# Kernel optimization log

Measured on AMD Instinct MI355X. Metric: run time of the kernel, lower is better.

The kernel has to match this reference:

```python
import jax, jax.numpy as jnp
import numpy as np
from functools import partial

NUM_HEADS = 12
RATIO_ACT = 0.5   # prune_ratio_act_store
RATIO_ATTN = 0.5  # prune_ratio_attn_mat_store


def kth_mask(x, ratio):
    # torch.kthvalue semantics: threshold = k-th SMALLEST of |x| over the flat tensor
    n = x.size
    k = int(np.clip(n * ratio, 1, n))
    mag = jnp.abs(x)
    thr = jnp.sort(mag.reshape(-1))[k - 1]
    return (mag >= thr).astype(x.dtype)


def st(dense, prune):
    # straight-through: value = dense, gradient flows through `prune` path
    return jax.lax.stop_gradient(dense) + prune - jax.lax.stop_gradient(prune)


def _softmax_prune_impl(x, ratio):
    dense = jax.nn.softmax(x, axis=-1)
    mask = kth_mask(dense, ratio)
    return dense, mask * dense


@partial(jax.custom_vjp, nondiff_argnums=(1,))
def softmax_prune(x, ratio):
    return _softmax_prune_impl(x, ratio)


def _sp_fwd(x, ratio):
    dense, sparse = _softmax_prune_impl(x, ratio)
    return (dense, sparse), sparse


def _sp_bwd(ratio, A, cots):
    # custom backward uses the SPARSE probs in the softmax Jacobian; the
    # cotangent of the sparse output is ignored (matches the torch Function)
    g_dense, _ = cots
    g = A * (g_dense - jnp.sum(g_dense * A, axis=-1, keepdims=True))
    return (g,)


softmax_prune.defvjp(_sp_fwd, _sp_bwd)


def setup_inputs() -> dict:
    key = jax.random.key(0)
    ks = jax.random.split(key, 5)
    B, S, H = 8, 577, 768
    hs = jax.random.normal(ks[0], (B, S, H), dtype=jnp.float32)
    w = lambda k: jax.random.normal(k, (H, H), dtype=jnp.float32) * 0.02
    z = jnp.zeros((H,), dtype=jnp.float32)
    return {
        "hidden_states": hs,
        "Wq": w(ks[1]), "bq": z,
        "Wk": w(ks[2]), "bk": z,
        "Wv": w(ks[3]), "bv": z,
        "Wo": w(ks[4]), "bo": z,
    }


def attention_forward(hidden_states, Wq, bq, Wk, bk, Wv, bv, Wo, bo):
    B, S, H = hidden_states.shape
    nh, hd = NUM_HEADS, H // NUM_HEADS
    sg = jax.lax.stop_gradient
    lin = lambda x, W, b: x @ W + b

    # prune hidden states by global magnitude threshold
    hs_p = sg(kth_mask(hidden_states, RATIO_ACT)) * hidden_states

    q = st(lin(hidden_states, Wq, bq), lin(hs_p, Wq, bq))
    k = st(lin(hidden_states, Wk, bk), lin(hs_p, Wk, bk))
    v = st(lin(hidden_states, Wv, bv), lin(hs_p, Wv, bv))

    heads = lambda x: x.reshape(B, S, nh, hd).transpose(0, 2, 1, 3)  # [B,h,S,d]
    q, k, v = heads(q), heads(k), heads(v)

    qp = sg(kth_mask(q, RATIO_ACT)) * q
    kp = sg(kth_mask(k, RATIO_ACT)) * k

    scores = st(jnp.einsum('bhqd,bhkd->bhqk', q, k),
                jnp.einsum('bhqd,bhkd->bhqk', qp, kp))
    scores = scores / float(np.sqrt(hd))

    probs, probs_p = softmax_prune(scores, RATIO_ATTN)  # dropout rate = 0 -> identity

    vp = sg(kth_mask(v, RATIO_ACT)) * v
    ctx = st(jnp.einsum('bhqk,bhkd->bhqd', probs, v),
             jnp.einsum('bhqk,bhkd->bhqd', probs_p, vp))

    ctx = ctx.transpose(0, 2, 1, 3).reshape(B, S, H)
    ctx_p = sg(kth_mask(ctx, RATIO_ACT)) * ctx

    out = st(lin(ctx, Wo, bo), lin(ctx_p, Wo, bo))
    return out  # vis=False -> weights is None


def reference(hidden_states, Wq, bq, Wk, bk, Wv, bv, Wo, bo):
    return attention_forward(hidden_states, Wq, bq, Wk, bk, Wv, bv, Wo, bo)
```

## Files before the change

### kernel.cpp

```cpp
#include <hip/hip_runtime.h>
#include <hip/hip_bf16.h>


#define B_ 8
#define S_ 577
#define H_ 768
#define NH_ 12
#define HD_ 64
#define M_ (B_*S_)
#define MPAD 4736
#define BH_ (B_*NH_)
#define SKPAD 640
#define LTS 136

typedef __attribute__((ext_vector_type(8))) short short8;
typedef __attribute__((ext_vector_type(4))) short s16x4;
typedef __attribute__((ext_vector_type(4))) float f32x4;

__device__ inline unsigned short f2bf(float f){
    unsigned int u = __float_as_uint(f);
    u = u + 0x7fffu + ((u>>16)&1u);
    return (unsigned short)(u>>16);
}

__device__ inline void gload_lds16(const short* g, short* l){
    __builtin_amdgcn_global_load_lds((const __attribute__((address_space(1))) void*)g,
                                     (__attribute__((address_space(3))) void*)l, 16, 0, 0);
}

__global__ __launch_bounds__(256) void k_prep(
    const float* __restrict__ hs, short* __restrict__ abf,
    const float* __restrict__ Wq, const float* __restrict__ Wk,
    const float* __restrict__ Wv, const float* __restrict__ Wo,
    short* __restrict__ Tq, short* __restrict__ Tk,
    short* __restrict__ Tv, short* __restrict__ To,
    short* __restrict__ kh, short* __restrict__ vt)
{
    const int bid = blockIdx.x, t = threadIdx.x;
    if(bid < 1776){
        int i = bid*256 + t;
        if(bid >= 1731){ *(short8*)(abf + (size_t)i*8) = (short8){}; return; }
        const float4* p = (const float4*)(hs + (size_t)i*8);
        float4 a = p[0], b = p[1];
        short8 v;
        v[0]=(short)f2bf(a.x); v[1]=(short)f2bf(a.y); v[2]=(short)f2bf(a.z); v[3]=(short)f2bf(a.w);
        v[4]=(short)f2bf(b.x); v[5]=(short)f2bf(b.y); v[6]=(short)f2bf(b.z); v[7]=(short)f2bf(b.w);
        *(short8*)(abf + (size_t)i*8) = v;
    } else if(bid < 2352){
        int zidx = bid - 1776;
        int z = zidx & 3, rem = zidx >> 2;
        int kx = rem % 12, ny = rem / 12;
        const float* W = z==0?Wq: z==1?Wk: z==2?Wv:Wo;
        short*       T = z==0?Tq: z==1?Tk: z==2?Tv:To;
        __shared__ float lds[64][65];
        int k0 = kx*64, n0 = ny*64;
        for(int i=0;i<4;i++){
            int row = i*16 + (t>>4);
            int col = (t&15)*4;
            float4 v = *(const float4*)&W[(k0+row)*768 + n0 + col];
            lds[row][col]=v.x; lds[row][col+1]=v.y; lds[row][col+2]=v.z; lds[row][col+3]=v.w;
        }
        __syncthreads();
        for(int i=0;i<4;i++){
            int n = i*16 + (t>>4);
            int k4 = (t&15)*4;
            for(int j=0;j<4;j++)
                T[(n0+n)*768 + k0 + k4 + j] = (short)f2bf(lds[k4+j][n]);
        }
    } else {
        int tid = (bid-2352)*256 + t;
        short8 z = {};
        if(tid < 48384){
            int row_id = tid>>3, ch = tid&7;
            int bh = row_id/63, r = row_id - bh*63;
            *(short8*)&kh[((size_t)bh*SKPAD + 577 + r)*64 + ch*8] = z;
        } else if(tid < 97536){
            int j = tid - 48384;
            int row_id = j>>3, ch = j&7;
            int bh = row_id>>6, d = row_id&63;
            *(short8*)&vt[((size_t)bh*64 + d)*SKPAD + 576 + ch*8] = z;
        }
    }
}

__global__ __launch_bounds__(512) void k_gemm(
    const short* __restrict__ A, const short* __restrict__ T,
    const float* __restrict__ b0, const float* __restrict__ b1, const float* __restrict__ b2,
    short* __restrict__ oq, short* __restrict__ ok, short* __restrict__ ovt,
    float* __restrict__ of, int mode, int NT)
{
    __shared__ short sh[32768];
    const int t = threadIdx.x;

    const int nwg = gridDim.x;
    const int q8 = nwg>>3, r8 = nwg&7;
    const int xcd = blockIdx.x&7, cidx = blockIdx.x>>3;
    const int wg = (xcd<r8 ? xcd*(q8+1) : r8*(q8+1) + (xcd-r8)*q8) + cidx;
    const int mt = wg/NT, ntile = wg - mt*NT;
    const int m0 = mt*128, n0 = ntile*128;

    const int seg = (mode==3)? 0 : n0/768;
    const float* bias = (mode==3)? b0 : (seg==0?b0: seg==1?b1:b2);
    const int nlb = (mode==3)? n0 : n0 - seg*768;

    const int w = t>>6, lane = t&63, g = lane>>4, c = lane&15;
    const int wm = w>>1, wn = w&1;

    const int lrow = lane>>3;
    const int lcol = ((lane&7) ^ lrow) * 8;
    const short* pa = A + (size_t)(m0 + w*8 + lrow)*768 + lcol;
    const short* pb = T + (size_t)(n0 + w*8 + lrow)*768 + lcol;

    f32x4 acc[2][4] = {};

    #pragma unroll
    for(int i=0;i<2;i++){
        gload_lds16(pa + (size_t)(i*64)*768, &sh[(i*64 + w*8)*64]);
        gload_lds16(pb + (size_t)(i*64)*768, &sh[8192 + (i*64 + w*8)*64]);
    }
    int bb = 0;
    for(int kk=0; kk<12; kk++){
        if(kk<11){
            short* dstA = &sh[(bb^1)*16384];
            short* dstB = dstA + 8192;
            #pragma unroll
            for(int i=0;i<2;i++){
                gload_lds16(pa + (size_t)(i*64)*768 + (kk+1)*64, &dstA[(i*64 + w*8)*64]);
                gload_lds16(pb + (size_t)(i*64)*768 + (kk+1)*64, &dstB[(i*64 + w*8)*64]);
            }
            asm volatile("s_waitcnt vmcnt(4)" ::: "memory");
        } else {
            asm volatile("s_waitcnt vmcnt(0)" ::: "memory");
        }
        __builtin_amdgcn_s_barrier();
        asm volatile("" ::: "memory");

        const short* LA = &sh[bb*16384];
        const short* LB = LA + 8192;
        short8 af[2][2], bfv[4][2];
        #pragma unroll
        for(int mi=0; mi<2; mi++){
            int row = wm*32 + mi*16 + c;
            int rx = (row&7)<<3;
            af[mi][0] = *(const short8*)&LA[row*64 + ((g*8) ^ rx)];
            af[mi][1] = *(const short8*)&LA[row*64 + ((32 + g*8) ^ rx)];
        }
        #pragma unroll
        for(int ni=0; ni<4; ni++){
            int row = wn*64 + ni*16 + c;
            int rx = (row&7)<<3;
            bfv[ni][0] = *(const short8*)&LB[row*64 + ((g*8) ^ rx)];
            bfv[ni][1] = *(const short8*)&LB[row*64 + ((32 + g*8) ^ rx)];
        }
        __builtin_amdgcn_s_setprio(1);
        #pragma unroll
        for(int mi=0; mi<2; mi++)
            #pragma unroll
            for(int ni=0; ni<4; ni++){
                acc[mi][ni] = __builtin_amdgcn_mfma_f32_16x16x32_bf16(af[mi][0], bfv[ni][0], acc[mi][ni], 0,0,0);
                acc[mi][ni] = __builtin_amdgcn_mfma_f32_16x16x32_bf16(af[mi][1], bfv[ni][1], acc[mi][ni], 0,0,0);
            }
        __builtin_amdgcn_s_setprio(0);
        asm volatile("s_waitcnt lgkmcnt(0)" ::: "memory");
        __builtin_amdgcn_s_barrier();
        asm volatile("" ::: "memory");
        bb ^= 1;
    }

    if(mode==3){
        #pragma unroll
        for(int mi=0; mi<2; mi++) for(int ni=0; ni<4; ni++){
            #pragma unroll
            for(int r=0; r<4; r++){
                int m = m0 + wm*32 + mi*16 + g*4 + r;
                int n = n0 + wn*64 + ni*16 + c;
                if(m >= M_) continue;
                of[(size_t)m*768 + n] = acc[mi][ni][r] + bias[n];
            }
        }
        return;
    }

    if(seg==2){
        #pragma unroll
        for(int mi=0;mi<2;mi++)
            #pragma unroll
            for(int ni=0;ni<4;ni++){
                int nl_ = wn*64 + ni*16 + c;
                float bv = bias[nlb + nl_];
                s16x4 pk;
                #pragma unroll
                for(int r=0;r<4;r++) pk[r] = (short)f2bf(acc[mi][ni][r] + bv);
                int ml0 = wm*32 + mi*16 + g*4;
                *(s16x4*)&sh[nl_*LTS + ml0] = pk;
            }
    } else {
        #pragma unroll
        for(int mi=0;mi<2;mi++)
            #pragma unroll
            for(int ni=0;ni<4;ni++){
                int nl_ = wn*64 + ni*16 + c;
                float bv = bias[nlb + nl_];
                #pragma unroll
                for(int r=0;r<4;r++){
                    int ml = wm*32 + mi*16 + g*4 + r;
                    sh[ml*LTS + nl_] = (short)f2bf(acc[mi][ni][r] + bv);
                }
            }
    }
    __syncthreads();

    #pragma unroll
    for(int i=0;i<4;i++){
        int idx = i*512 + t;
        int rp = idx>>4, ch = idx&15;
        short8 v8 = *(const short8*)&sh[rp*LTS + ch*8];
        if(seg==2){
            int nl = nlb + rp, hh = nl>>6, dd = nl&63;
            int mg = m0 + ch*8;
            if(mg < M_){
                int b0_ = mg/S_, s0 = mg - b0_*S_;
                if(s0+7 < S_ && mg+7 < M_){
                    *(short8*)&ovt[(((size_t)b0_*NH_+hh)*HD_+dd)*SKPAD + s0] = v8;
                } else {
                    for(int j=0;j<8;j++){
                        int m=mg+j;
                        if(m<M_){ int bj=m/S_, sj=m-bj*S_;
                            ovt[(((size_t)bj*NH_+hh)*HD_+dd)*SKPAD+sj]=v8[j]; }
                    }
                }
            }
        } else {
            int m = m0 + rp;
            if(m < M_){
                int b0_ = m/S_, s0 = m - b0_*S_;
                int nl = nlb + ch*8, hh = nl>>6, dd = nl&63;
                if(seg==1) *(short8*)&ok[(((size_t)b0_*NH_+hh)*SKPAD + s0)*HD_ + dd] = v8;
                else       *(short8*)&oq[(((size_t)b0_*NH_+hh)*S_   + s0)*HD_ + dd] = v8;
            }
        }
    }
}

__global__ __launch_bounds__(256) void k_attn(
    const short* __restrict__ qh, const short* __restrict__ kh, const short* __restrict__ vt,
    short* __restrict__ ctx)
{
    __shared__ short lP[4*2048];
    const int t = threadIdx.x;
    const int w = t>>6, lane = t&63, g = lane>>4, c = lane&15;
    const int bh = blockIdx.x, b = bh/NH_, h = bh%NH_;
    const int q0 = blockIdx.y*128;

    #pragma unroll
    for(int i=0;i<4;i++){
        int row = i*8 + (lane>>3);
        int e8 = (lane&7)*8;
        int s = q0 + w*32 + row;
        short8 v = {};
        if(s < S_) v = *(const short8*)&qh[((size_t)bh*S_ + s)*HD_ + e8];
        *(short8*)&lP[w*2048 + row*64 + (e8 ^ ((row&7)<<3))] = v;
    }
    short8 qf[2][2];
    #pragma unroll
    for(int qi=0; qi<2; qi++)
        #pragma unroll
        for(int ks=0; ks<2; ks++)
            qf[qi][ks] = *(const short8*)&lP[w*2048 + (qi*16+c)*64 + ((ks*32+g*8) ^ ((c&7)<<3))];

    short8 ones;
    #pragma unroll
    for(int j=0;j<8;j++) ones[j] = (short)0x3F80;

    const short* Kb = kh + (size_t)bh*SKPAD*64 + (size_t)c*64 + g*8;
    const short* Vb = vt + (size_t)bh*64*SKPAD + (size_t)c*SKPAD + g*8;

    float m_run[2][4], l_run[2][4];
    f32x4 O[2][4] = {};
    #pragma unroll
    for(int qi=0;qi<2;qi++)
        #pragma unroll
        for(int r=0;r<4;r++){ m_run[qi][r] = -3e38f; l_run[qi][r] = 0.f; }

    #pragma unroll 1
    for(int kt=0; kt<10; kt++){
        const int key0 = kt*64;
        short8 kf[4][2], vf[4][2];
        #pragma unroll
        for(int nt=0; nt<4; nt++){
            const short* kr = Kb + (size_t)(key0 + nt*16)*64;
            kf[nt][0] = *(const short8*)(kr);
            kf[nt][1] = *(const short8*)(kr + 32);
            const short* vr = Vb + (size_t)(nt*16)*SKPAD + key0;
            vf[nt][0] = *(const short8*)(vr);
            vf[nt][1] = *(const short8*)(vr + 32);
        }

        float sv[2][4][4];
        #pragma unroll
        for(int nt=0; nt<4; nt++){
            __builtin_amdgcn_s_setprio(1);
            #pragma unroll
            for(int qi=0; qi<2; qi++){
                f32x4 sa = {};
                sa = __builtin_amdgcn_mfma_f32_16x16x32_bf16(qf[qi][0], kf[nt][0], sa, 0,0,0);
                sa = __builtin_amdgcn_mfma_f32_16x16x32_bf16(qf[qi][1], kf[nt][1], sa, 0,0,0);
                #pragma unroll
                for(int r=0;r<4;r++) sv[qi][nt][r] = sa[r]*0.18033688011f;
            }
            __builtin_amdgcn_s_setprio(0);
        }
        if(kt==9){
            #pragma unroll
            for(int nt=0; nt<4; nt++){
                int key = 576 + nt*16 + c;
                if(key >= S_){
                    #pragma unroll
                    for(int qi=0;qi<2;qi++)
                        #pragma unroll
                        for(int r=0;r<4;r++) sv[qi][nt][r] = -3e38f;
                }
            }
        }
        float fac[2][4];
        #pragma unroll
        for(int qi=0; qi<2; qi++)
            #pragma unroll
            for(int r=0;r<4;r++){
                float mx = fmaxf(fmaxf(sv[qi][0][r],sv[qi][1][r]),fmaxf(sv[qi][2][r],sv[qi][3][r]));
                for(int off=1; off<16; off<<=1) mx = fmaxf(mx, __shfl_xor(mx, off));
                float nm = fmaxf(m_run[qi][r], mx);
                fac[qi][r] = __builtin_amdgcn_exp2f(m_run[qi][r] - nm);
                m_run[qi][r] = nm;
            }
        #pragma unroll
        for(int qi=0; qi<2; qi++)
            #pragma unroll
            for(int nt=0; nt<4; nt++)
                #pragma unroll
                for(int r=0;r<4;r++){
                    float p = __builtin_amdgcn_exp2f(sv[qi][nt][r] - m_run[qi][r]);
                    int prow = g*4 + r;
                    lP[w*2048 + qi*1024 + prow*64 + ((nt*16 + c) ^ ((prow&7)<<3))] = (short)f2bf(p);
                }
        short8 pf[2][2];
        #pragma unroll
        for(int qi=0; qi<2; qi++)
            #pragma unroll
            for(int ks=0; ks<2; ks++)
                pf[qi][ks] = *(const short8*)&lP[w*2048 + qi*1024 + c*64 + ((ks*32+g*8) ^ ((c&7)<<3))];
        __builtin_amdgcn_s_setprio(1);
        #pragma unroll
        for(int qi=0; qi<2; qi++){
            f32x4 rs = {};
            rs = __builtin_amdgcn_mfma_f32_16x16x32_bf16(pf[qi][0], ones, rs, 0,0,0);
            rs = __builtin_amdgcn_mfma_f32_16x16x32_bf16(pf[qi][1], ones, rs, 0,0,0);
            #pragma unroll
            for(int r=0;r<4;r++) l_run[qi][r] = l_run[qi][r]*fac[qi][r] + rs[r];
        }
        __builtin_amdgcn_s_setprio(0);
        #pragma unroll
        for(int qi=0; qi<2; qi++)
            #pragma unroll
            for(int nt=0;nt<4;nt++)
                #pragma unroll
                for(int r=0;r<4;r++) O[qi][nt][r] *= fac[qi][r];

        __builtin_amdgcn_s_setprio(1);
        #pragma unroll
        for(int nt=0; nt<4; nt++)
            #pragma unroll
            for(int qi=0; qi<2; qi++){
                O[qi][nt] = __builtin_amdgcn_mfma_f32_16x16x32_bf16(pf[qi][0], vf[nt][0], O[qi][nt], 0,0,0);
                O[qi][nt] = __builtin_amdgcn_mfma_f32_16x16x32_bf16(pf[qi][1], vf[nt][1], O[qi][nt], 0,0,0);
            }
        __builtin_amdgcn_s_setprio(0);
    }

    #pragma unroll
    for(int qi=0; qi<2; qi++)
        #pragma unroll
        for(int nt=0; nt<4; nt++)
            #pragma unroll
            for(int r=0;r<4;r++){
                int s = q0 + w*32 + qi*16 + g*4 + r;
                if(s < S_){
                    float val = O[qi][nt][r] / l_run[qi][r];
                    ctx[((size_t)b*S_ + s)*H_ + h*HD_ + nt*16 + c] = (short)f2bf(val);
                }
            }
}

extern "C" void kernel_launch(void* const* d_in, const int* in_sizes, int n_in,
                              void* d_out, int out_size, void* d_ws, size_t ws_size,
                              hipStream_t stream)
{
    const float* hs = (const float*)d_in[0];
    const float* Wq = (const float*)d_in[1];
    const float* bq = (const float*)d_in[2];
    const float* Wk = (const float*)d_in[3];
    const float* bk = (const float*)d_in[4];
    const float* Wv = (const float*)d_in[5];
    const float* bv = (const float*)d_in[6];
    const float* Wo = (const float*)d_in[7];
    const float* bo = (const float*)d_in[8];
    float* out = (float*)d_out;

    char* ws = (char*)d_ws;
    short* abf = (short*)(ws);
    short* ctx = abf;
    short* wqt = (short*)(ws + 7274496);
    short* wkt = (short*)(ws + 7274496 + 1179648);
    short* wvt = (short*)(ws + 7274496 + 2*1179648);
    short* wot = (short*)(ws + 7274496 + 3*1179648);
    short* qh  = (short*)(ws + 11993088);
    short* kh  = (short*)(ws + 19083264);
    short* vt  = (short*)(ws + 26947584);

    k_prep<<<2733, 256, 0, stream>>>(hs, abf, Wq,Wk,Wv,Wo, wqt,wkt,wvt,wot, kh, vt);
    k_gemm<<<666, 512, 0, stream>>>(abf, wqt, bq,bk,bv, qh,kh,vt, nullptr, 0, 18);
    k_attn<<<dim3(96,5), 256, 0, stream>>>(qh, kh, vt, ctx);
    k_gemm<<<222, 512, 0, stream>>>(ctx, wot, bo,bo,bo, nullptr,nullptr,nullptr, out, 3, 6);
}
```

Measured before the change: 102.3 us.

## Stage K/V tiles in double-buffered LDS with async global-to-LDS loads

The attention kernel now loads 128-key K and V tiles cooperatively into shared LDS with direct global-to-LDS loads. It double-buffers them so the next tile is fetched while the current one is computed, and the key loop drops from ten 64-key steps to five 128-key steps. The aim is to cut redundant per-wave global loads of K/V, since all four waves previously fetched the same data, and to hide memory latency. The cost is about 80KB of LDS per block plus extra barriers, which may lower occupancy.

```diff
diff --git a/kernel.cpp b/kernel.cpp
--- a/kernel.cpp
+++ b/kernel.cpp
@@ -246,7 +246,7 @@
     const short* __restrict__ qh, const short* __restrict__ kh, const short* __restrict__ vt,
     short* __restrict__ ctx)
 {
-    __shared__ short lP[4*2048];
+    __shared__ short lK[2][128*64], lV[2][64*128], lP[4*2048];
     const int t = threadIdx.x;
     const int w = t>>6, lane = t&63, g = lane>>4, c = lane&15;
     const int bh = blockIdx.x, b = bh/NH_, h = bh%NH_;
@@ -272,8 +272,22 @@
     #pragma unroll
     for(int j=0;j<8;j++) ones[j] = (short)0x3F80;
 
-    const short* Kb = kh + (size_t)bh*SKPAD*64 + (size_t)c*64 + g*8;
-    const short* Vb = vt + (size_t)bh*64*SKPAD + (size_t)c*SKPAD + g*8;
+    const short* pk[4]; const short* pv[4]; int dk[4], dv[4];
+    #pragma unroll
+    for(int i=0;i<4;i++){
+        int id = i*256 + t;
+        int krow = id>>3, kch = id&7;
+        pk[i] = kh + ((size_t)bh*SKPAD + krow)*64 + (kch ^ (krow&7))*8;
+        dk[i] = krow*64 + kch*8;
+        int vd = id>>4, vch = id&15;
+        pv[i] = vt + ((size_t)bh*64 + vd)*SKPAD + (vch ^ (vd&7))*8;
+        dv[i] = vd*128 + vch*8;
+    }
+    #define STAGE(kt) { _Pragma("unroll") for(int i_=0;i_<4;i_++){           \
+        gload_lds16(pk[i_] + (size_t)(kt)*8192, &lK[(kt)&1][dk[i_]]);        \
+        gload_lds16(pv[i_] + (kt)*128,          &lV[(kt)&1][dv[i_]]); } }
+
+    STAGE(0);
 
     float m_run[2][4], l_run[2][4];
     f32x4 O[2][4] = {};
@@ -282,100 +296,99 @@
         #pragma unroll
         for(int r=0;r<4;r++){ m_run[qi][r] = -3e38f; l_run[qi][r] = 0.f; }
 
-    #pragma unroll 1
-    for(int kt=0; kt<10; kt++){
-        const int key0 = kt*64;
-        short8 kf[4][2], vf[4][2];
-        #pragma unroll
-        for(int nt=0; nt<4; nt++){
-            const short* kr = Kb + (size_t)(key0 + nt*16)*64;
-            kf[nt][0] = *(const short8*)(kr);
-            kf[nt][1] = *(const short8*)(kr + 32);
-            const short* vr = Vb + (size_t)(nt*16)*SKPAD + key0;
-            vf[nt][0] = *(const short8*)(vr);
-            vf[nt][1] = *(const short8*)(vr + 32);
-        }
-
-        float sv[2][4][4];
-        #pragma unroll
-        for(int nt=0; nt<4; nt++){
-            __builtin_amdgcn_s_setprio(1);
-            #pragma unroll
-            for(int qi=0; qi<2; qi++){
+    for(int kt=0; kt<5; kt++){
+        if(kt<4){
+            STAGE(kt+1);
+            asm volatile("s_waitcnt vmcnt(8)" ::: "memory");
+        } else {
+            asm volatile("s_waitcnt vmcnt(0)" ::: "memory");
+        }
+        __builtin_amdgcn_s_barrier();
+        asm volatile("" ::: "memory");
+
+        const short* LK = lK[kt&1]; const short* LV = lV[kt&1];
+
+        #pragma unroll
+        for(int qi=0; qi<2; qi++){
+            float sv[8][4];
+            #pragma unroll
+            for(int nt=0; nt<8; nt++){
+                int row = nt*16 + c;
+                int rx = (row&7)<<3;
+                short8 kf0 = *(const short8*)&LK[row*64 + ((g*8) ^ rx)];
+                short8 kf1 = *(const short8*)&LK[row*64 + ((32+g*8) ^ rx)];
+                __builtin_amdgcn_s_setprio(1);
                 f32x4 sa = {};
-                sa = __builtin_amdgcn_mfma_f32_16x16x32_bf16(qf[qi][0], kf[nt][0], sa, 0,0,0);
-                sa = __builtin_amdgcn_mfma_f32_16x16x32_bf16(qf[qi][1], kf[nt][1], sa, 0,0,0);
-                #pragma unroll
-                for(int r=0;r<4;r++) sv[qi][nt][r] = sa[r]*0.18033688011f;
-            }
-            __builtin_amdgcn_s_setprio(0);
-        }
-        if(kt==9){
-            #pragma unroll
-            for(int nt=0; nt<4; nt++){
-                int key = 576 + nt*16 + c;
-                if(key >= S_){
-                    #pragma unroll
-                    for(int qi=0;qi<2;qi++)
+                sa = __builtin_amdgcn_mfma_f32_16x16x32_bf16(qf[qi][0], kf0, sa, 0,0,0);
+                sa = __builtin_amdgcn_mfma_f32_16x16x32_bf16(qf[qi][1], kf1, sa, 0,0,0);
+                __builtin_amdgcn_s_setprio(0);
+                #pragma unroll
+                for(int r=0;r<4;r++) sv[nt][r] = sa[r]*0.18033688011f;
+            }
+            if(kt==4){
+                #pragma unroll
+                for(int nt=0; nt<8; nt++){
+                    int key = 512 + nt*16 + c;
+                    if(key >= S_){
                         #pragma unroll
-                        for(int r=0;r<4;r++) sv[qi][nt][r] = -3e38f;
-                }
-            }
-        }
-        float fac[2][4];
-        #pragma unroll
-        for(int qi=0; qi<2; qi++)
+                        for(int r=0;r<4;r++) sv[nt][r] = -3e38f;
+                    }
+                }
+            }
+            float fac[4];
             #pragma unroll
             for(int r=0;r<4;r++){
-                float mx = fmaxf(fmaxf(sv[qi][0][r],sv[qi][1][r]),fmaxf(sv[qi][2][r],sv[qi][3][r]));
+                float mx = sv[0][r];
+                #pragma unroll
+                for(int nt=1;nt<8;nt++) mx = fmaxf(mx, sv[nt][r]);
                 for(int off=1; off<16; off<<=1) mx = fmaxf(mx, __shfl_xor(mx, off));
                 float nm = fmaxf(m_run[qi][r], mx);
-                fac[qi][r] = __builtin_amdgcn_exp2f(m_run[qi][r] - nm);
+                fac[r] = __builtin_amdgcn_exp2f(m_run[qi][r] - nm);
                 m_run[qi][r] = nm;
             }
-        #pragma unroll
-        for(int qi=0; qi<2; qi++)
-            #pragma unroll
-            for(int nt=0; nt<4; nt++)
+            #pragma unroll
+            for(int nt=0; nt<8; nt++)
                 #pragma unroll
                 for(int r=0;r<4;r++){
-                    float p = __builtin_amdgcn_exp2f(sv[qi][nt][r] - m_run[qi][r]);
+                    float p = __builtin_amdgcn_exp2f(sv[nt][r] - m_run[qi][r]);
                     int prow = g*4 + r;
-                    lP[w*2048 + qi*1024 + prow*64 + ((nt*16 + c) ^ ((prow&7)<<3))] = (short)f2bf(p);
-                }
-        short8 pf[2][2];
-        #pragma unroll
-        for(int qi=0; qi<2; qi++)
-            #pragma unroll
-            for(int ks=0; ks<2; ks++)
-                pf[qi][ks] = *(const short8*)&lP[w*2048 + qi*1024 + c*64 + ((ks*32+g*8) ^ ((c&7)<<3))];
-        __builtin_amdgcn_s_setprio(1);
-        #pragma unroll
-        for(int qi=0; qi<2; qi++){
+                    lP[w*2048 + prow*128 + ((nt*16 + c) ^ ((prow&7)<<3))] = (short)f2bf(p);
+                }
+            short8 pf[4];
+            #pragma unroll
+            for(int ks=0; ks<4; ks++)
+                pf[ks] = *(const short8*)&lP[w*2048 + c*128 + ((ks*32+g*8) ^ ((c&7)<<3))];
+            __builtin_amdgcn_s_setprio(1);
             f32x4 rs = {};
-            rs = __builtin_amdgcn_mfma_f32_16x16x32_bf16(pf[qi][0], ones, rs, 0,0,0);
-            rs = __builtin_amdgcn_mfma_f32_16x16x32_bf16(pf[qi][1], ones, rs, 0,0,0);
-            #pragma unroll
-            for(int r=0;r<4;r++) l_run[qi][r] = l_run[qi][r]*fac[qi][r] + rs[r];
-        }
-        __builtin_amdgcn_s_setprio(0);
-        #pragma unroll
-        for(int qi=0; qi<2; qi++)
+            #pragma unroll
+            for(int ks=0; ks<4; ks++)
+                rs = __builtin_amdgcn_mfma_f32_16x16x32_bf16(pf[ks], ones, rs, 0,0,0);
+            __builtin_amdgcn_s_setprio(0);
+            #pragma unroll
+            for(int r=0;r<4;r++) l_run[qi][r] = l_run[qi][r]*fac[r] + rs[r];
             #pragma unroll
             for(int nt=0;nt<4;nt++)
                 #pragma unroll
-                for(int r=0;r<4;r++) O[qi][nt][r] *= fac[qi][r];
-
-        __builtin_amdgcn_s_setprio(1);
-        #pragma unroll
-        for(int nt=0; nt<4; nt++)
-            #pragma unroll
-            for(int qi=0; qi<2; qi++){
-                O[qi][nt] = __builtin_amdgcn_mfma_f32_16x16x32_bf16(pf[qi][0], vf[nt][0], O[qi][nt], 0,0,0);
-                O[qi][nt] = __builtin_amdgcn_mfma_f32_16x16x32_bf16(pf[qi][1], vf[nt][1], O[qi][nt], 0,0,0);
-            }
-        __builtin_amdgcn_s_setprio(0);
-    }
+                for(int r=0;r<4;r++) O[qi][nt][r] *= fac[r];
+
+            __builtin_amdgcn_s_setprio(1);
+            #pragma unroll
+            for(int nt=0; nt<4; nt++){
+                int vrow = nt*16 + c;
+                int rx = (vrow&7)<<3;
+                #pragma unroll
+                for(int ks=0; ks<4; ks++){
+                    short8 vf = *(const short8*)&LV[vrow*128 + ((ks*32+g*8) ^ rx)];
+                    O[qi][nt] = __builtin_amdgcn_mfma_f32_16x16x32_bf16(pf[ks], vf, O[qi][nt], 0,0,0);
+                }
+            }
+            __builtin_amdgcn_s_setprio(0);
+        }
+        asm volatile("s_waitcnt lgkmcnt(0)" ::: "memory");
+        __builtin_amdgcn_s_barrier();
+        asm volatile("" ::: "memory");
+    }
+    #undef STAGE
 
     #pragma unroll
     for(int qi=0; qi<2; qi++)
```

Result: faster. 86.09 us (-15.9%).
